# Optimization experiments

Measured on AMD Instinct MI355X. Metric: run time of the kernel, lower is better.

## Reference

```python
import jax, jax.numpy as jnp
import numpy as np

T = 128          # number_of_trees
B = 1024         # batch_size
D = 28 * 28      # hardcoded feature dim
K = 200          # hardcoded top-k


def setup_inputs() -> dict:
    key = jax.random.key(0)
    k1, k2 = jax.random.split(key)
    x = jax.random.normal(k1, (B, D), dtype=jnp.float32)
    attention_mask = jax.random.uniform(k2, (T, D), dtype=jnp.float32, minval=-1.0, maxval=1.0)
    return {"x": x, "attention_mask": attention_mask}


def reference(x, attention_mask):
    # sigmoid -> top-k -> scatter builds a sparse per-tree mask [T, D]
    att = jax.nn.sigmoid(attention_mask)                      # [T, D]
    topk, idx = jax.lax.top_k(att, K)                         # [T, K] each
    rows = jnp.arange(T)[:, None]                             # [T, 1]
    attention = jnp.zeros((T, D), dtype=att.dtype).at[rows, idx].set(topk)  # [T, D]
    # per-tree broadcast multiply, vectorized (replaces python loop over trees)
    xf = x.reshape(-1, D)                                     # [B, D]
    return_value = xf[:, None, :] * attention[None, :, :]     # [B, T, D]
    return (return_value, attention)
```

## Files before the change

kernel.cpp:

```cpp
#include <hip/hip_runtime.h>
#include <math.h>

#define NT 128
#define NB 1024
#define ND 784
#define NK 200
#define ND4 196

typedef float vfloat4 __attribute__((ext_vector_type(4)));

__global__ __launch_bounds__(256) void topk_attention_kernel(
    const float* __restrict__ mask, float* __restrict__ att_out)
{
    __shared__ unsigned int su[ND];
    __shared__ float        sv[ND];
    __shared__ unsigned char sel[ND];
    __shared__ int          cnts[32];

    const int t   = blockIdx.x;
    const int tid = threadIdx.x;

    if (tid < 32) cnts[tid] = 0;

    for (int d = tid; d < ND; d += 256) {
        float f = mask[t * ND + d];
        unsigned int b = __float_as_uint(f);
        su[d]  = ((int)b < 0) ? ~b : (b | 0x80000000u);
        sv[d]  = 1.0f / (1.0f + expf(-f));
        sel[d] = 0;
    }
    __syncthreads();

    unsigned int p = 0;
    int need = NK;
    for (int bit = 31; bit >= 0; --bit) {
        const unsigned int test = (p | (1u << bit)) >> bit;
        int local = 0;
        for (int d = tid; d < ND; d += 256)
            local += ((su[d] >> bit) == test) ? 1 : 0;
        #pragma unroll
        for (int off = 32; off > 0; off >>= 1)
            local += __shfl_down(local, off);
        if ((tid & 63) == 0) atomicAdd(&cnts[bit], local);
        __syncthreads();
        const int c = cnts[bit];
        if (c >= need) p |= (1u << bit);
        else           need -= c;
    }

    for (int d = tid; d < ND; d += 256)
        sel[d] = (su[d] > p) ? 1 : 0;
    __syncthreads();
    if (tid == 0) {
        int rem = need;
        for (int d = 0; d < ND && rem > 0; ++d)
            if (su[d] == p) { sel[d] = 1; --rem; }
    }
    __syncthreads();

    for (int d = tid; d < ND; d += 256)
        att_out[t * ND + d] = sel[d] ? sv[d] : 0.0f;
}

__global__ __launch_bounds__(256) void bcast_mul_kernel(
    const vfloat4* __restrict__ x4, const vfloat4* __restrict__ att4,
    vfloat4* __restrict__ out4)
{
    __shared__ vfloat4 sx[ND4];
    const int b   = blockIdx.x;
    const int tid = threadIdx.x;
    if (tid < ND4) sx[tid] = x4[b * ND4 + tid];
    __syncthreads();

    vfloat4* __restrict__ outb = out4 + (size_t)b * (NT * ND4);
    #pragma unroll 2
    for (int i = tid; i < NT * ND4; i += 256) {
        const int t  = i / ND4;
        const int d4 = i - t * ND4;
        const vfloat4 av = att4[i];
        const vfloat4 xv = sx[d4];
        const vfloat4 o  = xv * av;
        __builtin_nontemporal_store(o, &outb[i]);
    }
}

extern "C" void kernel_launch(void* const* d_in, const int* in_sizes, int n_in,
                              void* d_out, int out_size, void* d_ws, size_t ws_size,
                              hipStream_t stream)
{
    (void)in_sizes; (void)n_in; (void)out_size; (void)d_ws; (void)ws_size;
    const float* x    = (const float*)d_in[0];
    const float* mask = (const float*)d_in[1];
    float* out = (float*)d_out;
    float* att = out + (size_t)NB * NT * ND;

    topk_attention_kernel<<<NT, 256, 0, stream>>>(mask, att);

    bcast_mul_kernel<<<NB, 256, 0, stream>>>(
        (const vfloat4*)x, (const vfloat4*)att, (vfloat4*)out);
}
```

Before: 483.7 us.

## Register-resident radix top-k and software-pipelined prefetch in broadcast multiply

The top-k kernel now keeps keys and sigmoid values in registers instead of shared memory. It replaces shared atomics with per-wave partial sums and resolves ties with ballot-based ranking rather than a serial single-thread scan. The broadcast-multiply kernel prefetches the next batch of attention vectors into registers while storing the current batch, and tracks the x index incrementally instead of dividing. This raises register use and hard-codes the loop trip counts to the problem shape.

```diff
diff --git a/kernel.cpp b/kernel.cpp
--- a/kernel.cpp
+++ b/kernel.cpp
@@ -6,60 +6,82 @@
 #define ND 784
 #define NK 200
 #define ND4 196
+#define UB 7
 
 typedef float vfloat4 __attribute__((ext_vector_type(4)));
 
 __global__ __launch_bounds__(256) void topk_attention_kernel(
     const float* __restrict__ mask, float* __restrict__ att_out)
 {
-    __shared__ unsigned int su[ND];
-    __shared__ float        sv[ND];
-    __shared__ unsigned char sel[ND];
-    __shared__ int          cnts[32];
+    __shared__ int wsum[32][4];
+    __shared__ int wtie[4][4];
 
-    const int t   = blockIdx.x;
-    const int tid = threadIdx.x;
+    const int t    = blockIdx.x;
+    const int tid  = threadIdx.x;
+    const int wave = tid >> 6;
+    const int lane = tid & 63;
 
-    if (tid < 32) cnts[tid] = 0;
-
-    for (int d = tid; d < ND; d += 256) {
-        float f = mask[t * ND + d];
-        unsigned int b = __float_as_uint(f);
-        su[d]  = ((int)b < 0) ? ~b : (b | 0x80000000u);
-        sv[d]  = 1.0f / (1.0f + expf(-f));
-        sel[d] = 0;
+    unsigned int key[4];
+    float        val[4];
+    #pragma unroll
+    for (int j = 0; j < 4; ++j) {
+        const int d = tid + j * 256;
+        if (d < ND) {
+            const float f = mask[t * ND + d];
+            const unsigned int b = __float_as_uint(f);
+            key[j] = ((int)b < 0) ? ~b : (b | 0x80000000u);
+            val[j] = 1.0f / (1.0f + expf(-f));
+        } else { key[j] = 0u; val[j] = 0.0f; }
     }
-    __syncthreads();
 
     unsigned int p = 0;
     int need = NK;
     for (int bit = 31; bit >= 0; --bit) {
-        const unsigned int test = (p | (1u << bit)) >> bit;
-        int local = 0;
-        for (int d = tid; d < ND; d += 256)
-            local += ((su[d] >> bit) == test) ? 1 : 0;
+        const unsigned int test = (p >> bit) | 1u;
+        int c = 0;
         #pragma unroll
-        for (int off = 32; off > 0; off >>= 1)
-            local += __shfl_down(local, off);
-        if ((tid & 63) == 0) atomicAdd(&cnts[bit], local);
+        for (int j = 0; j < 4; ++j) c += ((key[j] >> bit) == test) ? 1 : 0;
+        #pragma unroll
+        for (int off = 32; off > 0; off >>= 1) c += __shfl_down(c, off);
+        if (lane == 0) wsum[bit][wave] = c;
         __syncthreads();
-        const int c = cnts[bit];
-        if (c >= need) p |= (1u << bit);
-        else           need -= c;
+        const int tot = wsum[bit][0] + wsum[bit][1] + wsum[bit][2] + wsum[bit][3];
+        if (tot >= need) p |= (1u << bit);
+        else             need -= tot;
     }
 
-    for (int d = tid; d < ND; d += 256)
-        sel[d] = (su[d] > p) ? 1 : 0;
-    __syncthreads();
-    if (tid == 0) {
-        int rem = need;
-        for (int d = 0; d < ND && rem > 0; ++d)
-            if (su[d] == p) { sel[d] = 1; --rem; }
+    int rankw[4];
+    #pragma unroll
+    for (int j = 0; j < 4; ++j) {
+        const bool tie = (key[j] == p);
+        const unsigned long long m = __ballot(tie);
+        rankw[j] = __popcll(m & ((1ull << lane) - 1ull));
+        if (lane == 0) wtie[j][wave] = __popcll(m);
     }
     __syncthreads();
+    int jbase[4];
+    {
+        int pre = 0;
+        #pragma unroll
+        for (int j = 0; j < 4; ++j) {
+            jbase[j] = pre;
+            pre += wtie[j][0] + wtie[j][1] + wtie[j][2] + wtie[j][3];
+        }
+    }
 
-    for (int d = tid; d < ND; d += 256)
-        att_out[t * ND + d] = sel[d] ? sv[d] : 0.0f;
+    #pragma unroll
+    for (int j = 0; j < 4; ++j) {
+        const int d = tid + j * 256;
+        if (d < ND) {
+            bool keep = key[j] > p;
+            if (key[j] == p) {
+                int off = jbase[j] + rankw[j];
+                for (int w = 0; w < 4; ++w) if (w < wave) off += wtie[j][w];
+                keep = off < need;
+            }
+            att_out[t * ND + d] = keep ? val[j] : 0.0f;
+        }
+    }
 }
 
 __global__ __launch_bounds__(256) void bcast_mul_kernel(
@@ -73,14 +95,32 @@
     __syncthreads();
 
     vfloat4* __restrict__ outb = out4 + (size_t)b * (NT * ND4);
-    #pragma unroll 2
-    for (int i = tid; i < NT * ND4; i += 256) {
-        const int t  = i / ND4;
-        const int d4 = i - t * ND4;
-        const vfloat4 av = att4[i];
-        const vfloat4 xv = sx[d4];
-        const vfloat4 o  = xv * av;
-        __builtin_nontemporal_store(o, &outb[i]);
+
+    vfloat4 cur[UB];
+    #pragma unroll
+    for (int u = 0; u < UB; ++u) cur[u] = att4[tid + u * 256];
+
+    int d4 = (tid >= ND4) ? tid - ND4 : tid;
+
+    for (int nb = 0; nb < 13; ++nb) {
+        vfloat4 nxt[UB];
+        const int kb = nb * UB;
+        #pragma unroll
+        for (int u = 0; u < UB; ++u) nxt[u] = att4[tid + (kb + UB + u) * 256];
+        #pragma unroll
+        for (int u = 0; u < UB; ++u) {
+            const vfloat4 o = cur[u] * sx[d4];
+            __builtin_nontemporal_store(o, &outb[tid + (kb + u) * 256]);
+            d4 += 60; if (d4 >= ND4) d4 -= ND4;
+        }
+        #pragma unroll
+        for (int u = 0; u < UB; ++u) cur[u] = nxt[u];
+    }
+    #pragma unroll
+    for (int u = 0; u < UB; ++u) {
+        const vfloat4 o = cur[u] * sx[d4];
+        __builtin_nontemporal_store(o, &outb[tid + (13 * UB + u) * 256]);
+        d4 += 60; if (d4 >= ND4) d4 -= ND4;
     }
 }
 
@@ -95,7 +135,6 @@
     float* att = out + (size_t)NB * NT * ND;
 
     topk_attention_kernel<<<NT, 256, 0, stream>>>(mask, att);
-
     bcast_mul_kernel<<<NB, 256, 0, stream>>>(
         (const vfloat4*)x, (const vfloat4*)att, (vfloat4*)out);
 }
```

Result: faster. 421.8 us (-12.8%).
